# Optimization experiments

Hardware: AMD Instinct MI355X
Metric: run time of the kernel (lower is better)

The kernel has to match this reference:

```python
import jax, jax.numpy as jnp
import numpy as np

CONF_THRES = 0.1
IOU_THRES = 0.6
MAX_DET = 300
MAX_WH = 4096.0  # class offset for non-agnostic NMS
NEG_SLOPE = 0.01  # nn.LeakyReLU default


def xywh2xyxy(p):
    xy, wh = p[..., :2], p[..., 2:4]
    return jnp.concatenate([xy - wh / 2, xy + wh / 2], axis=-1)


def pairwise_iou(a, b):
    area_a = (a[:, 2] - a[:, 0]) * (a[:, 3] - a[:, 1])
    area_b = (b[:, 2] - b[:, 0]) * (b[:, 3] - b[:, 1])
    lt = jnp.maximum(a[:, None, :2], b[None, :, :2])
    rb = jnp.minimum(a[:, None, 2:], b[None, :, 2:])
    wh = jnp.clip(rb - lt, 0.0)
    inter = wh[..., 0] * wh[..., 1]
    return inter / (area_a[:, None] + area_b[None, :] - inter + 1e-7)


def nms_single(pred):  # pred: [N, 5+nc]
    boxes = xywh2xyxy(pred[:, :4])
    scores = pred[:, 5:] * pred[:, 4:5]  # obj * cls
    conf = jnp.max(scores, axis=1)
    cls = jnp.argmax(scores, axis=1)
    conf = jnp.where(conf > CONF_THRES, conf, 0.0)
    topv, topi = jax.lax.top_k(conf, MAX_DET)
    b = boxes[topi]                      # [K,4]
    c = cls[topi]
    valid = topv > CONF_THRES
    bo = b + (c.astype(b.dtype) * MAX_WH)[:, None]  # class-offset boxes
    iou = pairwise_iou(bo, bo)           # [K,K]
    idx = jnp.arange(MAX_DET)
    def body(i, keep):
        sup = keep[i] & (iou[i] > IOU_THRES) & (idx > i)
        return keep & ~sup
    keep = jax.lax.fori_loop(0, MAX_DET, body, valid)
    return b, keep


def bilinear_sample(feat, y, x):  # feat [C,H,W], y/x [K,P] -> [C,K,P]
    C, H, W = feat.shape
    y = jnp.clip(y, 0.0, H - 1.0)
    x = jnp.clip(x, 0.0, W - 1.0)
    y0 = jnp.floor(y).astype(jnp.int32)
    x0 = jnp.floor(x).astype(jnp.int32)
    y1 = jnp.minimum(y0 + 1, H - 1)
    x1 = jnp.minimum(x0 + 1, W - 1)
    ly = y - y0
    lx = x - x0
    return (feat[:, y0, x0] * ((1 - ly) * (1 - lx))
            + feat[:, y0, x1] * ((1 - ly) * lx)
            + feat[:, y1, x0] * (ly * (1 - lx))
            + feat[:, y1, x1] * (ly * lx))


def roi_align_1x1(feat, boxes, scale):  # feat [C,H,W], boxes [K,4] xyxy (input-px)
    b = boxes * scale
    w = jnp.maximum(b[:, 2] - b[:, 0], 1.0)
    h = jnp.maximum(b[:, 3] - b[:, 1], 1.0)
    off = jnp.array([0.5, 1.5], dtype=boxes.dtype)
    xs = b[:, 0:1] + off[None, :] * (w[:, None] / 2.0)  # [K,2]
    ys = b[:, 1:2] + off[None, :] * (h[:, None] / 2.0)
    yy = ys[:, jnp.array([0, 0, 1, 1])]  # [K,4] 2x2 grid
    xx = xs[:, jnp.array([0, 1, 0, 1])]
    v = bilinear_sample(feat, yy, xx)    # [C,K,4]
    return jnp.mean(v, axis=2).T         # [K,C]


def rescale_boxes(bbox, hw, hw0):  # scale_coords + normalize by orig shape
    gain = jnp.minimum(hw[0] / hw0[0], hw[1] / hw0[1])
    pad_x = (hw[1] - hw0[1] * gain) / 2.0
    pad_y = (hw[0] - hw0[0] * gain) / 2.0
    x1 = jnp.clip((bbox[:, 0] - pad_x) / gain, 0.0, hw0[1])
    y1 = jnp.clip((bbox[:, 1] - pad_y) / gain, 0.0, hw0[0])
    x2 = jnp.clip((bbox[:, 2] - pad_x) / gain, 0.0, hw0[1])
    y2 = jnp.clip((bbox[:, 3] - pad_y) / gain, 0.0, hw0[0])
    # divide by shapes[i][0] indexed [w,h,w,h]
    return jnp.stack([x1 / hw0[1], y1 / hw0[0], x2 / hw0[1], y2 / hw0[0]], axis=1)


def setup_inputs() -> dict:
    key = jax.random.key(0)
    ks = jax.random.split(key, 10)
    B, N, NC = 8, 25500, 80
    xy = jax.random.uniform(ks[0], (B, N, 2), minval=0.0, maxval=640.0)
    wh = jax.random.uniform(ks[1], (B, N, 2), minval=8.0, maxval=160.0)
    obj = jax.random.uniform(ks[2], (B, N, 1))
    cls = jax.random.uniform(ks[3], (B, N, NC))
    preds = jnp.concatenate([xy, wh, obj, cls], axis=-1)
    feat1 = jax.random.normal(ks[4], (B, 128, 80, 80), dtype=jnp.float32)
    feat2 = jax.random.normal(ks[5], (B, 256, 40, 40), dtype=jnp.float32)
    feat3 = jax.random.normal(ks[6], (B, 512, 20, 20), dtype=jnp.float32)
    feat4 = jax.random.normal(ks[7], (B, 1024, 10, 10), dtype=jnp.float32)
    orig_hw = jnp.tile(jnp.array([[720.0, 1280.0]], dtype=jnp.float32), (B, 1))
    W1 = jax.random.normal(ks[8], (1920, 256), dtype=jnp.float32) * 0.02
    b1 = jnp.zeros((256,), dtype=jnp.float32)
    W2 = jax.random.normal(ks[9], (256, 256), dtype=jnp.float32) * 0.02
    b2 = jnp.zeros((256,), dtype=jnp.float32)
    return {"preds": preds, "feat1": feat1, "feat2": feat2, "feat3": feat3,
            "feat4": feat4, "orig_hw": orig_hw, "W1": W1, "b1": b1,
            "W2": W2, "b2": b2}


def reference(preds, feat1, feat2, feat3, feat4, orig_hw, W1, b1, W2, b2):
    preds = jax.lax.stop_gradient(preds)  # out.detach() in the original
    hw = jnp.array(feat1.shape[-2:], dtype=preds.dtype) * 8.0  # network input h,w
    boxes, keep = jax.vmap(nms_single)(preds)  # [B,K,4], [B,K]
    f1 = jax.vmap(lambda f, b: roi_align_1x1(f, b, 1.0 / 8))(feat1, boxes)
    f2 = jax.vmap(lambda f, b: roi_align_1x1(f, b, 1.0 / 16))(feat2, boxes)
    f3 = jax.vmap(lambda f, b: roi_align_1x1(f, b, 1.0 / 32))(feat3, boxes)
    f4 = jax.vmap(lambda f, b: roi_align_1x1(f, b, 1.0 / 64))(feat4, boxes)
    f = jnp.concatenate([f1, f2, f3, f4], axis=-1)  # [B,K,1920]
    h = jax.nn.leaky_relu(f @ W1 + b1, NEG_SLOPE)
    h = jax.nn.leaky_relu(h @ W2 + b2, NEG_SLOPE)   # [B,K,256]
    bb = jax.vmap(lambda b, s: rescale_boxes(b, hw, s))(boxes, orig_hw)
    out = jnp.concatenate([bb, h], axis=-1)  # [B,K,260]
    return out * keep[..., None].astype(out.dtype)
```

## Files before the change

### kernel.cpp

```cpp
#include <hip/hip_runtime.h>
#include <hip/hip_bf16.h>
#include <cstdint>
#include <cstddef>

#define NBATCH 8
#define NANCH 25500
#define MAXDET 300

typedef __bf16 bf16x8 __attribute__((ext_vector_type(8)));
typedef float floatx4 __attribute__((ext_vector_type(4)));
typedef unsigned long long ull;

#define CONF_TILE 64
__global__ __launch_bounds__(256) void conf_kernel(const float* __restrict__ preds,
                                                   float* __restrict__ conf,
                                                   int* __restrict__ cls, int total) {
  __shared__ float s[CONF_TILE * 85];
  int base = blockIdx.x * CONF_TILE;
  int nA = total - base; if (nA > CONF_TILE) nA = CONF_TILE;
  int n4 = (nA * 85) >> 2;
  const float4* g4 = (const float4*)(preds + (size_t)base * 85);
  float4* s4 = (float4*)s;
  for (int i = threadIdx.x; i < n4; i += 256) s4[i] = g4[i];
  __syncthreads();
  int lane16 = threadIdx.x & 15;
  int sub = threadIdx.x >> 4;
  #pragma unroll
  for (int r = 0; r < 4; ++r) {
    int a = r * 16 + sub;
    if (a < nA) {
      const float* row = s + a * 85;
      float obj = row[4];
      float best = -1.0f; int bc = 0;
      #pragma unroll
      for (int j = 0; j < 5; ++j) {
        int c = lane16 * 5 + j;
        float v = row[5 + c] * obj;
        if (v > best) { best = v; bc = c; }
      }
      #pragma unroll
      for (int m = 1; m < 16; m <<= 1) {
        float ov = __shfl_xor(best, m, 64);
        int   oc = __shfl_xor(bc,   m, 64);
        if (ov > best || (ov == best && oc < bc)) { best = ov; bc = oc; }
      }
      if (lane16 == 0) {
        int idx = base + a;
        conf[idx] = (best > 0.1f) ? best : 0.0f;
        cls[idx] = bc;
      }
    }
  }
}

#define TK_CAP 2560
__global__ __launch_bounds__(1024) void topk_nms_kernel(const float* __restrict__ conf,
                                                        const float* __restrict__ preds,
                                                        const int* __restrict__ cls,
                                                        float* __restrict__ topv, int* __restrict__ topi,
                                                        float* __restrict__ cand_v, int* __restrict__ cand_i,
                                                        float* __restrict__ boxesWs, int* __restrict__ keepWs,
                                                        const float* __restrict__ orig_hw,
                                                        float* __restrict__ out, int N) {
  #pragma clang fp contract(off)
  __shared__ __align__(16) char smem[41216];
  int b = blockIdx.x;
  int t = threadIdx.x;

  {
    int* hist   = (int*)smem;
    int* spart  = (int*)(smem + 16384);
    float* lv_s = (float*)(smem + 20480);
    int* li_s   = (int*)(smem + 30720);
    int* shv    = (int*)(smem + 40960);
    const float* cf = conf + (size_t)b * N;
    const float4* cf4 = (const float4*)cf;
    int N4 = N >> 2;
    for (int i = t; i < 4096; i += 1024) hist[i] = 0;
    if (t == 0) { shv[0] = -1; shv[1] = 0; }
    __syncthreads();
    auto histo = [&](float v) {
      if (v > 0.1f) {
        unsigned bits = __float_as_uint(v);
        int bin = (int)((bits - 0x3D800000u) >> 13);
        if (bin > 4095) bin = 4095;
        atomicAdd(&hist[bin], 1);
      }
    };
    for (int i4 = t; i4 < N4; i4 += 1024) {
      float4 v = cf4[i4];
      histo(v.x); histo(v.y); histo(v.z); histo(v.w);
    }
    __syncthreads();
    int g = hist[4 * t] + hist[4 * t + 1] + hist[4 * t + 2] + hist[4 * t + 3];
    spart[t] = g;
    __syncthreads();
    for (int offs = 1; offs < 1024; offs <<= 1) {
      int v = (t + offs < 1024) ? spart[t + offs] : 0;
      __syncthreads();
      spart[t] += v;
      __syncthreads();
    }
    int total = spart[0];
    int target = total < 300 ? total : 300;
    if (total > 0) {
      int excl = spart[t] - g;
      int c3 = excl + hist[4 * t + 3];
      int c2 = c3 + hist[4 * t + 2];
      int c1 = c2 + hist[4 * t + 1];
      int c0 = c1 + hist[4 * t + 0];
      if      (c3 >= target) atomicMax(&shv[0], 4 * t + 3);
      else if (c2 >= target) atomicMax(&shv[0], 4 * t + 2);
      else if (c1 >= target) atomicMax(&shv[0], 4 * t + 1);
      else if (c0 >= target) atomicMax(&shv[0], 4 * t + 0);
    }
    __syncthreads();
    for (int i = t; i < 300; i += 1024) { topv[b * 300 + i] = 0.0f; topi[b * 300 + i] = 0; }
    int T = shv[0];
    float* cv = cand_v + (size_t)b * N;
    int* ci = cand_i + (size_t)b * N;
    if (total > 0) {
      auto cand = [&](float v, int idx) {
        if (v > 0.1f) {
          unsigned bits = __float_as_uint(v);
          int bin = (int)((bits - 0x3D800000u) >> 13);
          if (bin > 4095) bin = 4095;
          if (bin >= T) {
            int pos = atomicAdd(&shv[1], 1);
            if (pos < TK_CAP) { lv_s[pos] = v; li_s[pos] = idx; }
            else { cv[pos] = v; ci[pos] = idx; }
          }
        }
      };
      for (int i4 = t; i4 < N4; i4 += 1024) {
        float4 v = cf4[i4];
        int i = i4 * 4;
        cand(v.x, i); cand(v.y, i + 1); cand(v.z, i + 2); cand(v.w, i + 3);
      }
    }
    __syncthreads();
    int K = shv[1];
    int Klds = K < TK_CAP ? K : TK_CAP;
    for (int i = t; i < K; i += 1024) {
      float v; int id;
      if (i < TK_CAP) { v = lv_s[i]; id = li_s[i]; }
      else            { v = cv[i];   id = ci[i];   }
      int rank = 0;
      #pragma unroll 8
      for (int j = 0; j < Klds; ++j) {
        float vj = lv_s[j];
        int ij = li_s[j];
        int gt = vj > v;
        int eq = (vj == v) & (ij < id);
        rank += gt | eq;
      }
      for (int j = TK_CAP; j < K; ++j) {
        float vj = cv[j];
        int ij = ci[j];
        int gt = vj > v;
        int eq = (vj == v) & (ij < id);
        rank += gt | eq;
      }
      if (rank < 300) { topv[b * 300 + rank] = v; topi[b * 300 + rank] = id; }
    }
  }
  __syncthreads();

  {
    ull  (*mask)[5] = (ull(*)[5])smem;
    float (*bo5)[5] = (float(*)[5])(smem + 12032);
    float (*bxx)[4] = (float(*)[4])(smem + 18048);
    ull* keepw = (ull*)(smem + 22848);
    ull* nzrow = (ull*)(smem + 22888);
    if (t < 5) { keepw[t] = 0ULL; nzrow[t] = 0ULL; }
    __syncthreads();
    if (t < 300) {
      int i = topi[b * 300 + t];
      float v = topv[b * 300 + t];
      const float* p = preds + ((size_t)b * N + i) * 85;
      float cx = p[0], cy = p[1], w = p[2], h = p[3];
      float hw2 = w * 0.5f, hh2 = h * 0.5f;
      float x1 = cx - hw2, y1 = cy - hh2, x2 = cx + hw2, y2 = cy + hh2;
      bxx[t][0] = x1; bxx[t][1] = y1; bxx[t][2] = x2; bxx[t][3] = y2;
      size_t bi = ((size_t)(b * 300 + t)) * 4;
      boxesWs[bi + 0] = x1; boxesWs[bi + 1] = y1; boxesWs[bi + 2] = x2; boxesWs[bi + 3] = y2;
      int c = cls[(size_t)b * N + i];
      float off = (float)c * 4096.0f;
      float o0 = x1 + off, o1 = y1 + off, o2 = x2 + off, o3 = y2 + off;
      bo5[t][0] = o0; bo5[t][1] = o1; bo5[t][2] = o2; bo5[t][3] = o3;
      bo5[t][4] = (o2 - o0) * (o3 - o1);
      if (v > 0.1f) atomicOr(&keepw[t >> 6], 1ULL << (t & 63));
    }
    __syncthreads();
    {
      int wv = t >> 6, ln = t & 63;
      if (wv < 10) {
        int w = wv >> 1, half = wv & 1;
        int j = w * 64 + ln;
        int jc = j < 300 ? j : 0;
        float jb0 = bo5[jc][0], jb1 = bo5[jc][1], jb2 = bo5[jc][2], jb3 = bo5[jc][3], ja = bo5[jc][4];
        bool jv = j < 300;
        int iend = w * 64 + 64; if (iend > 300) iend = 300;
        int i0 = half * 150, i1 = i0 + 150; if (i1 > iend) i1 = iend;
        #pragma unroll 4
        for (int i = i0; i < i1; ++i) {
          float a0 = bo5[i][0], a1 = bo5[i][1], a2 = bo5[i][2], a3 = bo5[i][3], ai = bo5[i][4];
          float ltx = fmaxf(a0, jb0);
          float lty = fmaxf(a1, jb1);
          float rbx = fminf(a2, jb2);
          float rby = fminf(a3, jb3);
          float wx = fmaxf(rbx - ltx, 0.0f);
          float wy = fmaxf(rby - lty, 0.0f);
          float inter = wx * wy;
          float iou = inter / (ai + ja - inter + 1e-7f);
          ull bal = __ballot(jv && (j > i) && (iou > 0.6f));
          if (ln == 0) {
            mask[i][w] = bal;
            if (bal) atomicOr(&nzrow[i >> 6], 1ULL << (i & 63));
          }
        }
      }
    }
    __syncthreads();
    if (t == 0) {
      ull kw[5], nz[5];
      #pragma unroll
      for (int w = 0; w < 5; ++w) { kw[w] = keepw[w]; nz[w] = nzrow[w]; }
      #pragma unroll
      for (int w = 0; w < 5; ++w) {
        ull p = kw[w] & nz[w];
        while (p) {
          int l = __builtin_ctzll(p);
          p &= p - 1;
          int i = w * 64 + l;
          for (int w2 = w; w2 < 5; ++w2) {
            ull m = mask[i][w2];
            kw[w2] &= ~m;
            if (w2 == w) p &= ~m;
          }
        }
      }
      #pragma unroll
      for (int w = 0; w < 5; ++w) keepw[w] = kw[w];
    }
    __syncthreads();
    if (t < 300) {
      int kp = (int)((keepw[t >> 6] >> (t & 63)) & 1ULL);
      keepWs[b * 300 + t] = kp;
      float oh = orig_hw[b * 2 + 0], ow = orig_hw[b * 2 + 1];
      float gain = fminf(640.0f / oh, 640.0f / ow);
      float padx = (640.0f - ow * gain) * 0.5f;
      float pady = (640.0f - oh * gain) * 0.5f;
      float x1 = fminf(fmaxf((bxx[t][0] - padx) / gain, 0.0f), ow) / ow;
      float y1 = fminf(fmaxf((bxx[t][1] - pady) / gain, 0.0f), oh) / oh;
      float x2 = fminf(fmaxf((bxx[t][2] - padx) / gain, 0.0f), ow) / ow;
      float y2 = fminf(fmaxf((bxx[t][3] - pady) / gain, 0.0f), oh) / oh;
      size_t o = ((size_t)(b * 300 + t)) * 260;
      out[o + 0] = kp ? x1 : 0.0f;
      out[o + 1] = kp ? y1 : 0.0f;
      out[o + 2] = kp ? x2 : 0.0f;
      out[o + 3] = kp ? y2 : 0.0f;
    }
  }
}

struct TransArgs {
  const float* src[6];
  __hip_bfloat16* dst[6];
  int C[6], HW[6], tx[6], tpb[6], start[6];
};

__global__ void transpose_all_kernel(TransArgs a) {
  __shared__ float tile[32][33];
  int bid = blockIdx.x;
  int s = 0;
  #pragma unroll
  for (int i = 1; i < 6; ++i) if (bid >= a.start[i]) s = i;
  int local = bid - a.start[s];
  int C = a.C[s], HW = a.HW[s], tx0 = a.tx[s], tpb = a.tpb[s];
  int b = local / tpb;
  int rem = local - b * tpb;
  int p0 = (rem % tx0) * 32;
  int c0 = (rem / tx0) * 32;
  const float* inb = a.src[s] + (size_t)b * C * HW;
  __hip_bfloat16* outb = a.dst[s] + (size_t)b * C * HW;
  int tx = threadIdx.x, ty = threadIdx.y;
  #pragma unroll
  for (int k = 0; k < 32; k += 8) {
    int c = c0 + ty + k, p = p0 + tx;
    if (c < C && p < HW) tile[ty + k][tx] = inb[(size_t)c * HW + p];
  }
  __syncthreads();
  #pragma unroll
  for (int k = 0; k < 32; k += 8) {
    int p = p0 + ty + k, c = c0 + tx;
    if (p < HW && c < C) outb[(size_t)p * C + c] = __float2bfloat16(tile[tx][ty + k]);
  }
}

__global__ __launch_bounds__(256) void roi_kernel(const float* __restrict__ boxes,
                                                  const __hip_bfloat16* __restrict__ fT1, const __hip_bfloat16* __restrict__ fT2,
                                                  const __hip_bfloat16* __restrict__ fT3, const __hip_bfloat16* __restrict__ fT4,
                                                  __hip_bfloat16* __restrict__ f) {
  int b = blockIdx.x & 7;
  int r = blockIdx.x >> 3;
  __shared__ int t_off[4][16];
  __shared__ float t_w[4][16];
  int t = threadIdx.x;
  const int Hs[4] = {80, 40, 20, 10};
  const int Cs[4] = {128, 256, 512, 1024};
  const float ss[4] = {0.125f, 0.0625f, 0.03125f, 0.015625f};
  size_t bbase = ((size_t)(b * 300 + r)) * 4;
  float bx0 = boxes[bbase + 0];
  float by0 = boxes[bbase + 1];
  float bx1 = boxes[bbase + 2];
  float by1 = boxes[bbase + 3];
  if (t < 64) {
    int lv = t >> 4, k = t & 15, pp = k >> 2, nb = k & 3;
    float s = ss[lv];
    int H = Hs[lv], W = Hs[lv], C = Cs[lv];
    float b0 = bx0 * s, b1 = by0 * s, b2 = bx1 * s, b3 = by1 * s;
    float w = fmaxf(b2 - b0, 1.0f), h = fmaxf(b3 - b1, 1.0f);
    const float offv[2] = {0.5f, 1.5f};
    float px = b0 + offv[pp & 1] * (w * 0.5f);
    float py = b1 + offv[pp >> 1] * (h * 0.5f);
    float y = fminf(fmaxf(py, 0.0f), (float)(H - 1));
    float x = fminf(fmaxf(px, 0.0f), (float)(W - 1));
    int y0 = (int)floorf(y), x0 = (int)floorf(x);
    int y1 = min(y0 + 1, H - 1), x1 = min(x0 + 1, W - 1);
    float ly = y - (float)y0, lx = x - (float)x0;
    int yy = (nb & 2) ? y1 : y0;
    int xx = (nb & 1) ? x1 : x0;
    float wy = (nb & 2) ? ly : (1.0f - ly);
    float wx = (nb & 1) ? lx : (1.0f - lx);
    t_off[lv][k] = (yy * W + xx) * C;
    t_w[lv][k] = wy * wx;
  }
  __syncthreads();
  const __hip_bfloat16* bases[4] = {
    fT1 + (size_t)b * 6400 * 128,
    fT2 + (size_t)b * 1600 * 256,
    fT3 + (size_t)b * 400 * 512,
    fT4 + (size_t)b * 100 * 1024
  };
  __hip_bfloat16* frow = f + (size_t)(b * 300 + r) * 1920;
  int cbase = 0;
  #pragma unroll
  for (int lv = 0; lv < 4; ++lv) {
    int C = Cs[lv];
    const __hip_bfloat16* base = bases[lv];
    for (int c = t; c < C; c += 256) {
      float acc = 0.0f;
      #pragma unroll
      for (int k = 0; k < 16; ++k)
        acc += t_w[lv][k] * __bfloat162float(base[t_off[lv][k] + c]);
      frow[cbase + c] = __float2bfloat16(acc * 0.25f);
    }
    cbase += C;
  }
}

#define GLDS16(gp, lp) __builtin_amdgcn_global_load_lds( \
    (const __attribute__((address_space(1))) unsigned int*)(gp), \
    (__attribute__((address_space(3))) unsigned int*)(lp), 16, 0, 0)

__global__ __launch_bounds__(256) void gemm_tile_kernel(const __hip_bfloat16* __restrict__ A,
                                                        const __hip_bfloat16* __restrict__ BT,
                                                        const float* __restrict__ bias,
                                                        __hip_bfloat16* __restrict__ Cb,
                                                        float* __restrict__ Cf,
                                                        const int* __restrict__ keep,
                                                        int M, int N, int K, int ldc, int coff) {
  __shared__ __hip_bfloat16 sA[2][64 * 64];
  __shared__ __hip_bfloat16 sB[2][64 * 64];
  int tid = threadIdx.x;
  int bm = blockIdx.x * 64, bn = blockIdx.y * 64;
  int wave = tid >> 6, lane = tid & 63;
  int wr = wave >> 1, wc = wave & 1;
  int idx16 = lane & 15, kb = lane >> 4;
  floatx4 acc[2][2] = {};
  int nt = K >> 6;

  auto stage = [&](int buf, int t) {
    int k0 = t << 6;
    #pragma unroll
    for (int i = 0; i < 2; ++i) {
      int c = tid + i * 256;
      int row = c >> 3, cc = c & 7;
      int scc = cc ^ (row & 7);
      GLDS16(A + (size_t)(bm + row) * K + k0 + scc * 8,
             (char*)&sA[buf][0] + c * 16);
    }
    #pragma unroll
    for (int i = 0; i < 2; ++i) {
      int c = tid + i * 256;
      int row = c >> 3, cc = c & 7;
      int scc = cc ^ (row & 7);
      GLDS16(BT + (size_t)(bn + row) * K + k0 + scc * 8,
             (char*)&sB[buf][0] + c * 16);
    }
  };

  stage(0, 0);
  asm volatile("s_waitcnt vmcnt(0)" ::: "memory");
  __syncthreads();
  int cur = 0;
  for (int t = 0; t < nt; ++t) {
    if (t + 1 < nt) stage(cur ^ 1, t + 1);
    const char* Ab = (const char*)&sA[cur][0];
    const char* Bb = (const char*)&sB[cur][0];
    #pragma unroll
    for (int s = 0; s < 2; ++s) {
      bf16x8 af[2], bg[2];
      #pragma unroll
      for (int m = 0; m < 2; ++m) {
        int row = wr * 32 + m * 16 + idx16;
        int chunk = s * 4 + kb;
        af[m] = *(const bf16x8*)(Ab + row * 128 + ((chunk ^ (row & 7)) * 16));
      }
      #pragma unroll
      for (int n = 0; n < 2; ++n) {
        int row = wc * 32 + n * 16 + idx16;
        int chunk = s * 4 + kb;
        bg[n] = *(const bf16x8*)(Bb + row * 128 + ((chunk ^ (row & 7)) * 16));
      }
      #pragma unroll
      for (int m = 0; m < 2; ++m)
        #pragma unroll
        for (int n = 0; n < 2; ++n)
          acc[m][n] = __builtin_amdgcn_mfma_f32_16x16x32_bf16(af[m], bg[n], acc[m][n], 0, 0, 0);
    }
    asm volatile("s_waitcnt vmcnt(0)" ::: "memory");
    __syncthreads();
    cur ^= 1;
  }
  int col = lane & 15, rb4 = (lane >> 4) * 4;
  #pragma unroll
  for (int m = 0; m < 2; ++m) {
    #pragma unroll
    for (int n = 0; n < 2; ++n) {
      #pragma unroll
      for (int r = 0; r < 4; ++r) {
        int orow = bm + wr * 32 + m * 16 + rb4 + r;
        int ocol = bn + wc * 32 + n * 16 + col;
        if (orow >= M) continue;
        float v = acc[m][n][r] + bias[ocol];
        v = (v >= 0.0f) ? v : 0.01f * v;
        if (Cb) Cb[(size_t)orow * N + ocol] = __float2bfloat16(v);
        if (Cf) {
          float km = keep ? (keep[orow] ? 1.0f : 0.0f) : 1.0f;
          Cf[(size_t)orow * ldc + coff + ocol] = v * km;
        }
      }
    }
  }
}

extern "C" void kernel_launch(void* const* d_in, const int* in_sizes, int n_in,
                              void* d_out, int out_size, void* d_ws, size_t ws_size,
                              hipStream_t stream) {
  (void)in_sizes; (void)n_in; (void)out_size; (void)ws_size;
  const float* preds  = (const float*)d_in[0];
  const float* feat1  = (const float*)d_in[1];
  const float* feat2  = (const float*)d_in[2];
  const float* feat3  = (const float*)d_in[3];
  const float* feat4  = (const float*)d_in[4];
  const float* orighw = (const float*)d_in[5];
  const float* W1     = (const float*)d_in[6];
  const float* b1     = (const float*)d_in[7];
  const float* W2     = (const float*)d_in[8];
  const float* b2     = (const float*)d_in[9];
  float* out = (float*)d_out;

  char* ws = (char*)d_ws;
  size_t off = 0;
  auto alloc = [&](size_t bytes) -> void* {
    void* p = ws + off;
    off = (off + bytes + 255) & ~(size_t)255;
    return p;
  };
  const int BN = NBATCH * NANCH;
  float* conf   = (float*)alloc((size_t)BN * 4);
  int*   cls    = (int*)  alloc((size_t)BN * 4);
  float* cand_v = (float*)alloc((size_t)BN * 4);
  int*   cand_i = (int*)  alloc((size_t)BN * 4);
  float* topv   = (float*)alloc((size_t)NBATCH * 300 * 4);
  int*   topi   = (int*)  alloc((size_t)NBATCH * 300 * 4);
  float* boxes  = (float*)alloc((size_t)NBATCH * 300 * 4 * 4);
  int*   keep   = (int*)  alloc((size_t)NBATCH * 300 * 4);
  __hip_bfloat16* fT1  = (__hip_bfloat16*)alloc((size_t)NBATCH * 6400 * 128 * 2);
  __hip_bfloat16* fT2  = (__hip_bfloat16*)alloc((size_t)NBATCH * 1600 * 256 * 2);
  __hip_bfloat16* fT3  = (__hip_bfloat16*)alloc((size_t)NBATCH * 400 * 512 * 2);
  __hip_bfloat16* fT4  = (__hip_bfloat16*)alloc((size_t)NBATCH * 100 * 1024 * 2);
  __hip_bfloat16* fmat = (__hip_bfloat16*)alloc((size_t)2400 * 1920 * 2);
  __hip_bfloat16* h1b  = (__hip_bfloat16*)alloc((size_t)2400 * 256 * 2);
  __hip_bfloat16* W1T  = (__hip_bfloat16*)alloc((size_t)256 * 1920 * 2);
  __hip_bfloat16* W2T  = (__hip_bfloat16*)alloc((size_t)256 * 256 * 2);

  conf_kernel<<<(BN + CONF_TILE - 1) / CONF_TILE, 256, 0, stream>>>(preds, conf, cls, BN);
  topk_nms_kernel<<<NBATCH, 1024, 0, stream>>>(conf, preds, cls, topv, topi, cand_v, cand_i,
                                               boxes, keep, orighw, out, NANCH);
  TransArgs ta;
  ta.src[0] = feat1; ta.dst[0] = fT1; ta.C[0] = 128;  ta.HW[0] = 6400; ta.tx[0] = 200;
  ta.src[1] = feat2; ta.dst[1] = fT2; ta.C[1] = 256;  ta.HW[1] = 1600; ta.tx[1] = 50;
  ta.src[2] = feat3; ta.dst[2] = fT3; ta.C[2] = 512;  ta.HW[2] = 400;  ta.tx[2] = 13;
  ta.src[3] = feat4; ta.dst[3] = fT4; ta.C[3] = 1024; ta.HW[3] = 100;  ta.tx[3] = 4;
  ta.src[4] = W1;    ta.dst[4] = W1T; ta.C[4] = 1920; ta.HW[4] = 256;  ta.tx[4] = 8;
  ta.src[5] = W2;    ta.dst[5] = W2T; ta.C[5] = 256;  ta.HW[5] = 256;  ta.tx[5] = 8;
  int total_blocks = 0;
  for (int s = 0; s < 6; ++s) {
    int ty = (ta.C[s] + 31) / 32;
    int nbatch = (s < 4) ? NBATCH : 1;
    ta.tpb[s] = ta.tx[s] * ty;
    ta.start[s] = total_blocks;
    total_blocks += ta.tpb[s] * nbatch;
  }
  transpose_all_kernel<<<total_blocks, dim3(32, 8), 0, stream>>>(ta);
  roi_kernel<<<2400, 256, 0, stream>>>(boxes, fT1, fT2, fT3, fT4, fmat);
  gemm_tile_kernel<<<dim3(38, 4), 256, 0, stream>>>(fmat, W1T, b1, h1b, nullptr, nullptr,
                                                    2400, 256, 1920, 0, 0);
  gemm_tile_kernel<<<dim3(38, 4), 256, 0, stream>>>(h1b, W2T, b2, nullptr, out, keep,
                                                    2400, 256, 256, 260, 4);
}
```

Before: 142.5 us.

## Move top-k histogram into parallel blocks of transpose kernel, coarsen bins

The confidence histogram used for top-k threshold selection is now built by 64 extra blocks added to the transpose kernel (8 segments per batch), which accumulate into a global 512-bin histogram via atomics. The top-k/NMS kernel then only loads that histogram and does a wave-shuffle suffix scan, replacing the 4096-bin in-kernel histogram and the barrier-heavy scan. Top-k values and indices now stay in shared memory instead of a global scratch round trip. Coarser bins can admit more candidates for the rank pass, and TK_CAP is lowered to 2048, so more candidates may spill to global memory. The change also adds a memset launch.

```diff
diff --git a/kernel.cpp b/kernel.cpp
--- a/kernel.cpp
+++ b/kernel.cpp
@@ -53,78 +53,75 @@
   }
 }
 
-#define TK_CAP 2560
+#define TK_CAP 2048
 __global__ __launch_bounds__(1024) void topk_nms_kernel(const float* __restrict__ conf,
                                                         const float* __restrict__ preds,
                                                         const int* __restrict__ cls,
-                                                        float* __restrict__ topv, int* __restrict__ topi,
+                                                        const int* __restrict__ ghist,
                                                         float* __restrict__ cand_v, int* __restrict__ cand_i,
                                                         float* __restrict__ boxesWs, int* __restrict__ keepWs,
                                                         const float* __restrict__ orig_hw,
                                                         float* __restrict__ out, int N) {
   #pragma clang fp contract(off)
-  __shared__ __align__(16) char smem[41216];
+  __shared__ __align__(16) char smem[43008];
   int b = blockIdx.x;
   int t = threadIdx.x;
 
+  int*   s_h  = (int*)smem;
+  int*   s_c  = (int*)(smem + 2048);
+  float* tv   = (float*)(smem + 23040);
+  int*   ti   = (int*)(smem + 24256);
+  float* lv_s = (float*)(smem + 25600);
+  int*   li_s = (int*)(smem + 33792);
+  int*   shv  = (int*)(smem + 41984);
+
+  int T, total;
   {
-    int* hist   = (int*)smem;
-    int* spart  = (int*)(smem + 16384);
-    float* lv_s = (float*)(smem + 20480);
-    int* li_s   = (int*)(smem + 30720);
-    int* shv    = (int*)(smem + 40960);
+    if (t == 0) shv[1] = 0;
+    if (t < 512) s_h[t] = ghist[b * 512 + t];
+    for (int i = t; i < 300; i += 1024) { tv[i] = 0.0f; ti[i] = 0; }
+    __syncthreads();
+    int suff = 0;
+    if (t < 512) {
+      suff = s_h[t];
+      int l = t & 63;
+      #pragma unroll
+      for (int d = 1; d < 64; d <<= 1) {
+        int o = __shfl_down(suff, d, 64);
+        if (l + d < 64) suff += o;
+      }
+    }
+    __syncthreads();
+    if (t < 512 && (t & 63) == 0) s_h[t >> 6] = suff;
+    __syncthreads();
+    if (t < 512) {
+      int w = t >> 6;
+      int hi = 0;
+      #pragma unroll
+      for (int w2 = 1; w2 < 8; ++w2) if (w2 > w) hi += s_h[w2];
+      s_c[t] = suff + hi;
+    }
+    __syncthreads();
+    total = s_c[0];
+    int target = total < 300 ? total : 300;
+    if (t < 512) {
+      int c = s_c[t];
+      if (c >= target && (t == 511 || s_c[t + 1] < target)) shv[0] = t;
+    }
+    __syncthreads();
+    T = shv[0];
+
     const float* cf = conf + (size_t)b * N;
     const float4* cf4 = (const float4*)cf;
     int N4 = N >> 2;
-    for (int i = t; i < 4096; i += 1024) hist[i] = 0;
-    if (t == 0) { shv[0] = -1; shv[1] = 0; }
-    __syncthreads();
-    auto histo = [&](float v) {
-      if (v > 0.1f) {
-        unsigned bits = __float_as_uint(v);
-        int bin = (int)((bits - 0x3D800000u) >> 13);
-        if (bin > 4095) bin = 4095;
-        atomicAdd(&hist[bin], 1);
-      }
-    };
-    for (int i4 = t; i4 < N4; i4 += 1024) {
-      float4 v = cf4[i4];
-      histo(v.x); histo(v.y); histo(v.z); histo(v.w);
-    }
-    __syncthreads();
-    int g = hist[4 * t] + hist[4 * t + 1] + hist[4 * t + 2] + hist[4 * t + 3];
-    spart[t] = g;
-    __syncthreads();
-    for (int offs = 1; offs < 1024; offs <<= 1) {
-      int v = (t + offs < 1024) ? spart[t + offs] : 0;
-      __syncthreads();
-      spart[t] += v;
-      __syncthreads();
-    }
-    int total = spart[0];
-    int target = total < 300 ? total : 300;
-    if (total > 0) {
-      int excl = spart[t] - g;
-      int c3 = excl + hist[4 * t + 3];
-      int c2 = c3 + hist[4 * t + 2];
-      int c1 = c2 + hist[4 * t + 1];
-      int c0 = c1 + hist[4 * t + 0];
-      if      (c3 >= target) atomicMax(&shv[0], 4 * t + 3);
-      else if (c2 >= target) atomicMax(&shv[0], 4 * t + 2);
-      else if (c1 >= target) atomicMax(&shv[0], 4 * t + 1);
-      else if (c0 >= target) atomicMax(&shv[0], 4 * t + 0);
-    }
-    __syncthreads();
-    for (int i = t; i < 300; i += 1024) { topv[b * 300 + i] = 0.0f; topi[b * 300 + i] = 0; }
-    int T = shv[0];
     float* cv = cand_v + (size_t)b * N;
     int* ci = cand_i + (size_t)b * N;
     if (total > 0) {
       auto cand = [&](float v, int idx) {
         if (v > 0.1f) {
           unsigned bits = __float_as_uint(v);
-          int bin = (int)((bits - 0x3D800000u) >> 13);
-          if (bin > 4095) bin = 4095;
+          int bin = (int)((bits - 0x3D800000u) >> 16);
+          if (bin > 511) bin = 511;
           if (bin >= T) {
             int pos = atomicAdd(&shv[1], 1);
             if (pos < TK_CAP) { lv_s[pos] = v; li_s[pos] = idx; }
@@ -161,7 +158,7 @@
         int eq = (vj == v) & (ij < id);
         rank += gt | eq;
       }
-      if (rank < 300) { topv[b * 300 + rank] = v; topi[b * 300 + rank] = id; }
+      if (rank < 300) { tv[rank] = v; ti[rank] = id; }
     }
   }
   __syncthreads();
@@ -175,8 +172,8 @@
     if (t < 5) { keepw[t] = 0ULL; nzrow[t] = 0ULL; }
     __syncthreads();
     if (t < 300) {
-      int i = topi[b * 300 + t];
-      float v = topv[b * 300 + t];
+      int i = ti[t];
+      float v = tv[t];
       const float* p = preds + ((size_t)b * N + i) * 85;
       float cx = p[0], cy = p[1], w = p[2], h = p[3];
       float hw2 = w * 0.5f, hh2 = h * 0.5f;
@@ -270,9 +267,39 @@
   int C[6], HW[6], tx[6], tpb[6], start[6];
 };
 
-__global__ void transpose_all_kernel(TransArgs a) {
-  __shared__ float tile[32][33];
+__global__ void transpose_all_kernel(TransArgs a, const float* __restrict__ conf,
+                                     int* __restrict__ ghist, int hist_start) {
+  __shared__ __align__(16) char msm[4352];
   int bid = blockIdx.x;
+  if (bid >= hist_start) {
+    int* sh = (int*)msm;
+    int hb = bid - hist_start;
+    int b = hb >> 3, seg = hb & 7;
+    int tid = threadIdx.y * 32 + threadIdx.x;
+    sh[tid] = 0; sh[tid + 256] = 0;
+    __syncthreads();
+    const int N4 = NANCH >> 2;
+    int i0 = (N4 * seg) >> 3, i1 = (N4 * (seg + 1)) >> 3;
+    const float4* cf4 = (const float4*)(conf + (size_t)b * NANCH);
+    auto histo = [&](float v) {
+      if (v > 0.1f) {
+        unsigned bits = __float_as_uint(v);
+        int bin = (int)((bits - 0x3D800000u) >> 16);
+        if (bin > 511) bin = 511;
+        atomicAdd(&sh[bin], 1);
+      }
+    };
+    for (int i = i0 + tid; i < i1; i += 256) {
+      float4 v = cf4[i];
+      histo(v.x); histo(v.y); histo(v.z); histo(v.w);
+    }
+    __syncthreads();
+    int c0 = sh[tid], c1 = sh[tid + 256];
+    if (c0) atomicAdd(&ghist[b * 512 + tid], c0);
+    if (c1) atomicAdd(&ghist[b * 512 + tid + 256], c1);
+    return;
+  }
+  float (*tile)[33] = (float(*)[33])msm;
   int s = 0;
   #pragma unroll
   for (int i = 1; i < 6; ++i) if (bid >= a.start[i]) s = i;
@@ -484,8 +511,7 @@
   int*   cls    = (int*)  alloc((size_t)BN * 4);
   float* cand_v = (float*)alloc((size_t)BN * 4);
   int*   cand_i = (int*)  alloc((size_t)BN * 4);
-  float* topv   = (float*)alloc((size_t)NBATCH * 300 * 4);
-  int*   topi   = (int*)  alloc((size_t)NBATCH * 300 * 4);
+  int*   ghist  = (int*)  alloc((size_t)NBATCH * 512 * 4);
   float* boxes  = (float*)alloc((size_t)NBATCH * 300 * 4 * 4);
   int*   keep   = (int*)  alloc((size_t)NBATCH * 300 * 4);
   __hip_bfloat16* fT1  = (__hip_bfloat16*)alloc((size_t)NBATCH * 6400 * 128 * 2);
@@ -497,9 +523,10 @@
   __hip_bfloat16* W1T  = (__hip_bfloat16*)alloc((size_t)256 * 1920 * 2);
   __hip_bfloat16* W2T  = (__hip_bfloat16*)alloc((size_t)256 * 256 * 2);
 
+  hipMemsetAsync(ghist, 0, (size_t)NBATCH * 512 * 4, stream);
+
   conf_kernel<<<(BN + CONF_TILE - 1) / CONF_TILE, 256, 0, stream>>>(preds, conf, cls, BN);
-  topk_nms_kernel<<<NBATCH, 1024, 0, stream>>>(conf, preds, cls, topv, topi, cand_v, cand_i,
-                                               boxes, keep, orighw, out, NANCH);
+
   TransArgs ta;
   ta.src[0] = feat1; ta.dst[0] = fT1; ta.C[0] = 128;  ta.HW[0] = 6400; ta.tx[0] = 200;
   ta.src[1] = feat2; ta.dst[1] = fT2; ta.C[1] = 256;  ta.HW[1] = 1600; ta.tx[1] = 50;
@@ -515,7 +542,10 @@
     ta.start[s] = total_blocks;
     total_blocks += ta.tpb[s] * nbatch;
   }
-  transpose_all_kernel<<<total_blocks, dim3(32, 8), 0, stream>>>(ta);
+  transpose_all_kernel<<<total_blocks + 64, dim3(32, 8), 0, stream>>>(ta, conf, ghist, total_blocks);
+
+  topk_nms_kernel<<<NBATCH, 1024, 0, stream>>>(conf, preds, cls, ghist, cand_v, cand_i,
+                                               boxes, keep, orighw, out, NANCH);
   roi_kernel<<<2400, 256, 0, stream>>>(boxes, fT1, fT2, fT3, fT4, fmat);
   gemm_tile_kernel<<<dim3(38, 4), 256, 0, stream>>>(fmat, W1T, b1, h1b, nullptr, nullptr,
                                                     2400, 256, 1920, 0, 0);
```

Result: no change. 144.3 us (+1.2%).

## Overlap top-k candidate selection with transposes and bucket candidates by histogram bin

Applied to the files above, without the earlier changes.

The 8-block histogram/threshold/candidate-gather stage moves into the first blocks of the transpose kernel, so it runs alongside the feature and weight transposes instead of as a serial 8-block launch. Candidates are scattered into bin-sorted slots using suffix-sum counters, and each candidate's box and class are gathered at that point. Ranking then only compares against entries in the same bin instead of all candidates. The histogram becomes coarser (2048 bins), which can enlarge the threshold bin, and the scatter costs extra global writes of boxes and classes.

```diff
diff --git a/kernel.cpp b/kernel.cpp
--- a/kernel.cpp
+++ b/kernel.cpp
@@ -6,10 +6,17 @@
 #define NBATCH 8
 #define NANCH 25500
 #define MAXDET 300
+#define NBINS 2048
 
 typedef __bf16 bf16x8 __attribute__((ext_vector_type(8)));
 typedef float floatx4 __attribute__((ext_vector_type(4)));
 typedef unsigned long long ull;
+
+__device__ __forceinline__ int conf_bin(float v) {
+  unsigned bits = __float_as_uint(v);
+  int bin = (int)((bits - 0x3D800000u) >> 14);
+  return bin > (NBINS - 1) ? (NBINS - 1) : bin;
+}
 
 #define CONF_TILE 64
 __global__ __launch_bounds__(256) void conf_kernel(const float* __restrict__ preds,
@@ -53,226 +60,112 @@
   }
 }
 
-#define TK_CAP 2560
-__global__ __launch_bounds__(1024) void topk_nms_kernel(const float* __restrict__ conf,
-                                                        const float* __restrict__ preds,
-                                                        const int* __restrict__ cls,
-                                                        float* __restrict__ topv, int* __restrict__ topi,
-                                                        float* __restrict__ cand_v, int* __restrict__ cand_i,
-                                                        float* __restrict__ boxesWs, int* __restrict__ keepWs,
-                                                        const float* __restrict__ orig_hw,
-                                                        float* __restrict__ out, int N) {
-  #pragma clang fp contract(off)
-  __shared__ __align__(16) char smem[41216];
-  int b = blockIdx.x;
-  int t = threadIdx.x;
-
-  {
-    int* hist   = (int*)smem;
-    int* spart  = (int*)(smem + 16384);
-    float* lv_s = (float*)(smem + 20480);
-    int* li_s   = (int*)(smem + 30720);
-    int* shv    = (int*)(smem + 40960);
-    const float* cf = conf + (size_t)b * N;
-    const float4* cf4 = (const float4*)cf;
-    int N4 = N >> 2;
-    for (int i = t; i < 4096; i += 1024) hist[i] = 0;
-    if (t == 0) { shv[0] = -1; shv[1] = 0; }
-    __syncthreads();
-    auto histo = [&](float v) {
-      if (v > 0.1f) {
-        unsigned bits = __float_as_uint(v);
-        int bin = (int)((bits - 0x3D800000u) >> 13);
-        if (bin > 4095) bin = 4095;
-        atomicAdd(&hist[bin], 1);
-      }
-    };
-    for (int i4 = t; i4 < N4; i4 += 1024) {
-      float4 v = cf4[i4];
-      histo(v.x); histo(v.y); histo(v.z); histo(v.w);
-    }
-    __syncthreads();
-    int g = hist[4 * t] + hist[4 * t + 1] + hist[4 * t + 2] + hist[4 * t + 3];
-    spart[t] = g;
-    __syncthreads();
-    for (int offs = 1; offs < 1024; offs <<= 1) {
-      int v = (t + offs < 1024) ? spart[t + offs] : 0;
-      __syncthreads();
-      spart[t] += v;
-      __syncthreads();
-    }
-    int total = spart[0];
-    int target = total < 300 ? total : 300;
-    if (total > 0) {
-      int excl = spart[t] - g;
-      int c3 = excl + hist[4 * t + 3];
-      int c2 = c3 + hist[4 * t + 2];
-      int c1 = c2 + hist[4 * t + 1];
-      int c0 = c1 + hist[4 * t + 0];
-      if      (c3 >= target) atomicMax(&shv[0], 4 * t + 3);
-      else if (c2 >= target) atomicMax(&shv[0], 4 * t + 2);
-      else if (c1 >= target) atomicMax(&shv[0], 4 * t + 1);
-      else if (c0 >= target) atomicMax(&shv[0], 4 * t + 0);
-    }
-    __syncthreads();
-    for (int i = t; i < 300; i += 1024) { topv[b * 300 + i] = 0.0f; topi[b * 300 + i] = 0; }
-    int T = shv[0];
-    float* cv = cand_v + (size_t)b * N;
-    int* ci = cand_i + (size_t)b * N;
-    if (total > 0) {
-      auto cand = [&](float v, int idx) {
-        if (v > 0.1f) {
-          unsigned bits = __float_as_uint(v);
-          int bin = (int)((bits - 0x3D800000u) >> 13);
-          if (bin > 4095) bin = 4095;
-          if (bin >= T) {
-            int pos = atomicAdd(&shv[1], 1);
-            if (pos < TK_CAP) { lv_s[pos] = v; li_s[pos] = idx; }
-            else { cv[pos] = v; ci[pos] = idx; }
-          }
-        }
-      };
-      for (int i4 = t; i4 < N4; i4 += 1024) {
-        float4 v = cf4[i4];
-        int i = i4 * 4;
-        cand(v.x, i); cand(v.y, i + 1); cand(v.z, i + 2); cand(v.w, i + 3);
-      }
-    }
-    __syncthreads();
-    int K = shv[1];
-    int Klds = K < TK_CAP ? K : TK_CAP;
-    for (int i = t; i < K; i += 1024) {
-      float v; int id;
-      if (i < TK_CAP) { v = lv_s[i]; id = li_s[i]; }
-      else            { v = cv[i];   id = ci[i];   }
-      int rank = 0;
-      #pragma unroll 8
-      for (int j = 0; j < Klds; ++j) {
-        float vj = lv_s[j];
-        int ij = li_s[j];
-        int gt = vj > v;
-        int eq = (vj == v) & (ij < id);
-        rank += gt | eq;
-      }
-      for (int j = TK_CAP; j < K; ++j) {
-        float vj = cv[j];
-        int ij = ci[j];
-        int gt = vj > v;
-        int eq = (vj == v) & (ij < id);
-        rank += gt | eq;
-      }
-      if (rank < 300) { topv[b * 300 + rank] = v; topi[b * 300 + rank] = id; }
-    }
-  }
-  __syncthreads();
-
-  {
-    ull  (*mask)[5] = (ull(*)[5])smem;
-    float (*bo5)[5] = (float(*)[5])(smem + 12032);
-    float (*bxx)[4] = (float(*)[4])(smem + 18048);
-    ull* keepw = (ull*)(smem + 22848);
-    ull* nzrow = (ull*)(smem + 22888);
-    if (t < 5) { keepw[t] = 0ULL; nzrow[t] = 0ULL; }
-    __syncthreads();
-    if (t < 300) {
-      int i = topi[b * 300 + t];
-      float v = topv[b * 300 + t];
-      const float* p = preds + ((size_t)b * N + i) * 85;
-      float cx = p[0], cy = p[1], w = p[2], h = p[3];
-      float hw2 = w * 0.5f, hh2 = h * 0.5f;
-      float x1 = cx - hw2, y1 = cy - hh2, x2 = cx + hw2, y2 = cy + hh2;
-      bxx[t][0] = x1; bxx[t][1] = y1; bxx[t][2] = x2; bxx[t][3] = y2;
-      size_t bi = ((size_t)(b * 300 + t)) * 4;
-      boxesWs[bi + 0] = x1; boxesWs[bi + 1] = y1; boxesWs[bi + 2] = x2; boxesWs[bi + 3] = y2;
-      int c = cls[(size_t)b * N + i];
-      float off = (float)c * 4096.0f;
-      float o0 = x1 + off, o1 = y1 + off, o2 = x2 + off, o3 = y2 + off;
-      bo5[t][0] = o0; bo5[t][1] = o1; bo5[t][2] = o2; bo5[t][3] = o3;
-      bo5[t][4] = (o2 - o0) * (o3 - o1);
-      if (v > 0.1f) atomicOr(&keepw[t >> 6], 1ULL << (t & 63));
-    }
-    __syncthreads();
-    {
-      int wv = t >> 6, ln = t & 63;
-      if (wv < 10) {
-        int w = wv >> 1, half = wv & 1;
-        int j = w * 64 + ln;
-        int jc = j < 300 ? j : 0;
-        float jb0 = bo5[jc][0], jb1 = bo5[jc][1], jb2 = bo5[jc][2], jb3 = bo5[jc][3], ja = bo5[jc][4];
-        bool jv = j < 300;
-        int iend = w * 64 + 64; if (iend > 300) iend = 300;
-        int i0 = half * 150, i1 = i0 + 150; if (i1 > iend) i1 = iend;
-        #pragma unroll 4
-        for (int i = i0; i < i1; ++i) {
-          float a0 = bo5[i][0], a1 = bo5[i][1], a2 = bo5[i][2], a3 = bo5[i][3], ai = bo5[i][4];
-          float ltx = fmaxf(a0, jb0);
-          float lty = fmaxf(a1, jb1);
-          float rbx = fminf(a2, jb2);
-          float rby = fminf(a3, jb3);
-          float wx = fmaxf(rbx - ltx, 0.0f);
-          float wy = fmaxf(rby - lty, 0.0f);
-          float inter = wx * wy;
-          float iou = inter / (ai + ja - inter + 1e-7f);
-          ull bal = __ballot(jv && (j > i) && (iou > 0.6f));
-          if (ln == 0) {
-            mask[i][w] = bal;
-            if (bal) atomicOr(&nzrow[i >> 6], 1ULL << (i & 63));
-          }
-        }
-      }
-    }
-    __syncthreads();
-    if (t == 0) {
-      ull kw[5], nz[5];
-      #pragma unroll
-      for (int w = 0; w < 5; ++w) { kw[w] = keepw[w]; nz[w] = nzrow[w]; }
-      #pragma unroll
-      for (int w = 0; w < 5; ++w) {
-        ull p = kw[w] & nz[w];
-        while (p) {
-          int l = __builtin_ctzll(p);
-          p &= p - 1;
-          int i = w * 64 + l;
-          for (int w2 = w; w2 < 5; ++w2) {
-            ull m = mask[i][w2];
-            kw[w2] &= ~m;
-            if (w2 == w) p &= ~m;
-          }
-        }
-      }
-      #pragma unroll
-      for (int w = 0; w < 5; ++w) keepw[w] = kw[w];
-    }
-    __syncthreads();
-    if (t < 300) {
-      int kp = (int)((keepw[t >> 6] >> (t & 63)) & 1ULL);
-      keepWs[b * 300 + t] = kp;
-      float oh = orig_hw[b * 2 + 0], ow = orig_hw[b * 2 + 1];
-      float gain = fminf(640.0f / oh, 640.0f / ow);
-      float padx = (640.0f - ow * gain) * 0.5f;
-      float pady = (640.0f - oh * gain) * 0.5f;
-      float x1 = fminf(fmaxf((bxx[t][0] - padx) / gain, 0.0f), ow) / ow;
-      float y1 = fminf(fmaxf((bxx[t][1] - pady) / gain, 0.0f), oh) / oh;
-      float x2 = fminf(fmaxf((bxx[t][2] - padx) / gain, 0.0f), ow) / ow;
-      float y2 = fminf(fmaxf((bxx[t][3] - pady) / gain, 0.0f), oh) / oh;
-      size_t o = ((size_t)(b * 300 + t)) * 260;
-      out[o + 0] = kp ? x1 : 0.0f;
-      out[o + 1] = kp ? y1 : 0.0f;
-      out[o + 2] = kp ? x2 : 0.0f;
-      out[o + 3] = kp ? y2 : 0.0f;
-    }
-  }
-}
-
 struct TransArgs {
   const float* src[6];
   __hip_bfloat16* dst[6];
   int C[6], HW[6], tx[6], tpb[6], start[6];
 };
 
-__global__ void transpose_all_kernel(TransArgs a) {
-  __shared__ float tile[32][33];
+__global__ void transpose_all_kernel(TransArgs a,
+                                     const float* __restrict__ conf,
+                                     const float* __restrict__ preds,
+                                     const int* __restrict__ clsg,
+                                     float2* __restrict__ svid,
+                                     float4* __restrict__ sbox,
+                                     int* __restrict__ scls,
+                                     int* __restrict__ sufG,
+                                     int* __restrict__ tinfo) {
+  __shared__ __align__(16) char msm[17536];
   int bid = blockIdx.x;
+  if (bid < NBATCH) {
+    #pragma clang fp contract(off)
+    int b = bid;
+    int tid = threadIdx.y * 32 + threadIdx.x;
+    int* s_h   = (int*)msm;
+    int* s_ctr = (int*)(msm + 8192);
+    int* s_p   = (int*)(msm + 16384);
+    int* shv   = (int*)(msm + 17408);
+    for (int i = tid; i < NBINS; i += 256) s_h[i] = 0;
+    __syncthreads();
+    const float* cf = conf + (size_t)b * NANCH;
+    const float4* cf4 = (const float4*)cf;
+    const int N4 = NANCH >> 2;
+    for (int i = tid; i < N4; i += 256) {
+      float4 v = cf4[i];
+      if (v.x > 0.1f) atomicAdd(&s_h[conf_bin(v.x)], 1);
+      if (v.y > 0.1f) atomicAdd(&s_h[conf_bin(v.y)], 1);
+      if (v.z > 0.1f) atomicAdd(&s_h[conf_bin(v.z)], 1);
+      if (v.w > 0.1f) atomicAdd(&s_h[conf_bin(v.w)], 1);
+    }
+    __syncthreads();
+    int base = tid * 8;
+    int vals[8]; int ctot = 0;
+    #pragma unroll
+    for (int k = 0; k < 8; ++k) { vals[k] = s_h[base + k]; ctot += vals[k]; }
+    s_p[tid] = ctot;
+    __syncthreads();
+    for (int off = 1; off < 256; off <<= 1) {
+      int v = (tid + off < 256) ? s_p[tid + off] : 0;
+      __syncthreads();
+      s_p[tid] += v;
+      __syncthreads();
+    }
+    int total = s_p[0];
+    int above = (tid < 255) ? s_p[tid + 1] : 0;
+    int run = above;
+    #pragma unroll
+    for (int k = 7; k >= 0; --k) { run += vals[k]; s_h[base + k] = run; }
+    if (tid == 0) { sufG[b * (NBINS + 1) + NBINS] = 0; shv[0] = NBINS; }
+    __syncthreads();
+    int target = total < 300 ? total : 300;
+    int* sg = sufG + b * (NBINS + 1);
+    #pragma unroll
+    for (int k = 0; k < 8; ++k) {
+      int bin = base + k;
+      int sv = s_h[bin];
+      int nx = (bin < NBINS - 1) ? s_h[bin + 1] : 0;
+      s_ctr[bin] = nx;
+      sg[bin] = sv;
+      if (total > 0 && sv >= target && nx < target) shv[0] = bin;
+    }
+    __syncthreads();
+    int T = shv[0];
+    if (tid == 0) {
+      tinfo[b * 2 + 0] = total;
+      tinfo[b * 2 + 1] = (T < NBINS) ? s_h[T] : 0;
+    }
+    if (total > 0) {
+      float2* vb = svid + (size_t)b * NANCH;
+      float4* bb = sbox + (size_t)b * NANCH;
+      int*    cb = scls + (size_t)b * NANCH;
+      for (int i4 = tid; i4 < N4; i4 += 256) {
+        float4 v4 = cf4[i4];
+        int i0 = i4 * 4;
+        float vv[4] = {v4.x, v4.y, v4.z, v4.w};
+        #pragma unroll
+        for (int q = 0; q < 4; ++q) {
+          float v = vv[q];
+          if (v > 0.1f) {
+            int bin = conf_bin(v);
+            if (bin >= T) {
+              int slot = atomicAdd(&s_ctr[bin], 1);
+              int idx = i0 + q;
+              const float* p = preds + ((size_t)b * NANCH + idx) * 85;
+              float cx = p[0], cy = p[1], w = p[2], h = p[3];
+              float hw2 = w * 0.5f, hh2 = h * 0.5f;
+              float2 vi; vi.x = v; vi.y = __int_as_float(idx);
+              vb[slot] = vi;
+              float4 bx; bx.x = cx - hw2; bx.y = cy - hh2; bx.z = cx + hw2; bx.w = cy + hh2;
+              bb[slot] = bx;
+              cb[slot] = clsg[(size_t)b * NANCH + idx];
+            }
+          }
+        }
+      }
+    }
+    return;
+  }
+  float (*tile)[33] = (float(*)[33])msm;
   int s = 0;
   #pragma unroll
   for (int i = 1; i < 6; ++i) if (bid >= a.start[i]) s = i;
@@ -295,6 +188,149 @@
   for (int k = 0; k < 32; k += 8) {
     int p = p0 + ty + k, c = c0 + tx;
     if (p < HW && c < C) outb[(size_t)p * C + c] = __float2bfloat16(tile[tx][ty + k]);
+  }
+}
+
+__global__ __launch_bounds__(1024) void nms_kernel(const float2* __restrict__ svid,
+                                                   const float4* __restrict__ sbox,
+                                                   const int* __restrict__ scls,
+                                                   const int* __restrict__ sufG,
+                                                   const int* __restrict__ tinfo,
+                                                   float* __restrict__ boxesWs, int* __restrict__ keepWs,
+                                                   const float* __restrict__ orig_hw,
+                                                   float* __restrict__ out) {
+  #pragma clang fp contract(off)
+  __shared__ float4 bo4[300];
+  __shared__ float bxx[300][4];
+  __shared__ ull mask[300][5];
+  __shared__ ull keepw[5];
+  __shared__ ull nzrow[5];
+  int b = blockIdx.x;
+  int t = threadIdx.x;
+  int total  = tinfo[b * 2 + 0];
+  int Kslots = tinfo[b * 2 + 1];
+  int nvalid = total < 300 ? total : 300;
+
+  if (t < 300) {
+    bo4[t] = make_float4(0.0f, 0.0f, 0.0f, 0.0f);
+    bxx[t][0] = 0.0f; bxx[t][1] = 0.0f; bxx[t][2] = 0.0f; bxx[t][3] = 0.0f;
+    if (t >= nvalid) {
+      size_t bi = ((size_t)(b * 300 + t)) * 4;
+      boxesWs[bi + 0] = 0.0f; boxesWs[bi + 1] = 0.0f;
+      boxesWs[bi + 2] = 0.0f; boxesWs[bi + 3] = 0.0f;
+    }
+  }
+  if (t < 5) {
+    int kbase = t * 64;
+    int n = nvalid - kbase;
+    keepw[t] = (n <= 0) ? 0ULL : (n >= 64 ? ~0ULL : ((1ULL << n) - 1ULL));
+    nzrow[t] = 0ULL;
+  }
+  __syncthreads();
+
+  {
+    const float2* vb = svid + (size_t)b * NANCH;
+    const float4* bb = sbox + (size_t)b * NANCH;
+    const int*    cb = scls + (size_t)b * NANCH;
+    const int*   suf = sufG + b * (NBINS + 1);
+    for (int sIdx = t; sIdx < Kslots; sIdx += 1024) {
+      float2 vi = vb[sIdx];
+      float v = vi.x;
+      int id = __float_as_int(vi.y);
+      int bin = conf_bin(v);
+      int lo = suf[bin + 1], hi = suf[bin];
+      int rank = lo;
+      for (int j = lo; j < hi; ++j) {
+        float2 o = vb[j];
+        float vj = o.x;
+        int ij = __float_as_int(o.y);
+        rank += (int)((vj > v) | ((vj == v) & (ij < id)));
+      }
+      if (rank < 300) {
+        float4 bx = bb[sIdx];
+        int c = cb[sIdx];
+        float off = (float)c * 4096.0f;
+        float4 ob; ob.x = bx.x + off; ob.y = bx.y + off; ob.z = bx.z + off; ob.w = bx.w + off;
+        bo4[rank] = ob;
+        bxx[rank][0] = bx.x; bxx[rank][1] = bx.y; bxx[rank][2] = bx.z; bxx[rank][3] = bx.w;
+        size_t bi = ((size_t)(b * 300 + rank)) * 4;
+        boxesWs[bi + 0] = bx.x; boxesWs[bi + 1] = bx.y;
+        boxesWs[bi + 2] = bx.z; boxesWs[bi + 3] = bx.w;
+      }
+    }
+  }
+  __syncthreads();
+
+  {
+    int wv = t >> 6, ln = t & 63;
+    if (wv < 10) {
+      int w = wv >> 1, half = wv & 1;
+      int j = w * 64 + ln;
+      int jc = j < 300 ? j : 0;
+      float4 jb = bo4[jc];
+      float ja = (jb.z - jb.x) * (jb.w - jb.y);
+      bool jv = j < 300;
+      int iend = w * 64 + 64; if (iend > 300) iend = 300;
+      int i0 = half * 150, i1 = i0 + 150; if (i1 > iend) i1 = iend;
+      #pragma unroll 4
+      for (int i = i0; i < i1; ++i) {
+        float4 ib = bo4[i];
+        float ai = (ib.z - ib.x) * (ib.w - ib.y);
+        float ltx = fmaxf(ib.x, jb.x);
+        float lty = fmaxf(ib.y, jb.y);
+        float rbx = fminf(ib.z, jb.z);
+        float rby = fminf(ib.w, jb.w);
+        float wx = fmaxf(rbx - ltx, 0.0f);
+        float wy = fmaxf(rby - lty, 0.0f);
+        float inter = wx * wy;
+        float iou = inter / (ai + ja - inter + 1e-7f);
+        ull bal = __ballot(jv && (j > i) && (iou > 0.6f));
+        if (ln == 0) {
+          mask[i][w] = bal;
+          if (bal) atomicOr(&nzrow[i >> 6], 1ULL << (i & 63));
+        }
+      }
+    }
+  }
+  __syncthreads();
+  if (t == 0) {
+    ull kw[5], nz[5];
+    #pragma unroll
+    for (int w = 0; w < 5; ++w) { kw[w] = keepw[w]; nz[w] = nzrow[w]; }
+    #pragma unroll
+    for (int w = 0; w < 5; ++w) {
+      ull p = kw[w] & nz[w];
+      while (p) {
+        int l = __builtin_ctzll(p);
+        p &= p - 1;
+        int i = w * 64 + l;
+        for (int w2 = w; w2 < 5; ++w2) {
+          ull m = mask[i][w2];
+          kw[w2] &= ~m;
+          if (w2 == w) p &= ~m;
+        }
+      }
+    }
+    #pragma unroll
+    for (int w = 0; w < 5; ++w) keepw[w] = kw[w];
+  }
+  __syncthreads();
+  if (t < 300) {
+    int kp = (int)((keepw[t >> 6] >> (t & 63)) & 1ULL);
+    keepWs[b * 300 + t] = kp;
+    float oh = orig_hw[b * 2 + 0], ow = orig_hw[b * 2 + 1];
+    float gain = fminf(640.0f / oh, 640.0f / ow);
+    float padx = (640.0f - ow * gain) * 0.5f;
+    float pady = (640.0f - oh * gain) * 0.5f;
+    float x1 = fminf(fmaxf((bxx[t][0] - padx) / gain, 0.0f), ow) / ow;
+    float y1 = fminf(fmaxf((bxx[t][1] - pady) / gain, 0.0f), oh) / oh;
+    float x2 = fminf(fmaxf((bxx[t][2] - padx) / gain, 0.0f), ow) / ow;
+    float y2 = fminf(fmaxf((bxx[t][3] - pady) / gain, 0.0f), oh) / oh;
+    size_t o = ((size_t)(b * 300 + t)) * 260;
+    out[o + 0] = kp ? x1 : 0.0f;
+    out[o + 1] = kp ? y1 : 0.0f;
+    out[o + 2] = kp ? x2 : 0.0f;
+    out[o + 3] = kp ? y2 : 0.0f;
   }
 }
 
@@ -480,14 +516,15 @@
     return p;
   };
   const int BN = NBATCH * NANCH;
-  float* conf   = (float*)alloc((size_t)BN * 4);
-  int*   cls    = (int*)  alloc((size_t)BN * 4);
-  float* cand_v = (float*)alloc((size_t)BN * 4);
-  int*   cand_i = (int*)  alloc((size_t)BN * 4);
-  float* topv   = (float*)alloc((size_t)NBATCH * 300 * 4);
-  int*   topi   = (int*)  alloc((size_t)NBATCH * 300 * 4);
-  float* boxes  = (float*)alloc((size_t)NBATCH * 300 * 4 * 4);
-  int*   keep   = (int*)  alloc((size_t)NBATCH * 300 * 4);
+  float*  conf  = (float*)alloc((size_t)BN * 4);
+  int*    cls   = (int*)  alloc((size_t)BN * 4);
+  float2* svid  = (float2*)alloc((size_t)BN * 8);
+  float4* sbox  = (float4*)alloc((size_t)BN * 16);
+  int*    scls  = (int*)  alloc((size_t)BN * 4);
+  int*    sufG  = (int*)  alloc((size_t)NBATCH * (NBINS + 1) * 4);
+  int*    tinfo = (int*)  alloc((size_t)NBATCH * 2 * 4);
+  float*  boxes = (float*)alloc((size_t)NBATCH * 300 * 4 * 4);
+  int*    keep  = (int*)  alloc((size_t)NBATCH * 300 * 4);
   __hip_bfloat16* fT1  = (__hip_bfloat16*)alloc((size_t)NBATCH * 6400 * 128 * 2);
   __hip_bfloat16* fT2  = (__hip_bfloat16*)alloc((size_t)NBATCH * 1600 * 256 * 2);
   __hip_bfloat16* fT3  = (__hip_bfloat16*)alloc((size_t)NBATCH * 400 * 512 * 2);
@@ -498,8 +535,7 @@
   __hip_bfloat16* W2T  = (__hip_bfloat16*)alloc((size_t)256 * 256 * 2);
 
   conf_kernel<<<(BN + CONF_TILE - 1) / CONF_TILE, 256, 0, stream>>>(preds, conf, cls, BN);
-  topk_nms_kernel<<<NBATCH, 1024, 0, stream>>>(conf, preds, cls, topv, topi, cand_v, cand_i,
-                                               boxes, keep, orighw, out, NANCH);
+
   TransArgs ta;
   ta.src[0] = feat1; ta.dst[0] = fT1; ta.C[0] = 128;  ta.HW[0] = 6400; ta.tx[0] = 200;
   ta.src[1] = feat2; ta.dst[1] = fT2; ta.C[1] = 256;  ta.HW[1] = 1600; ta.tx[1] = 50;
@@ -507,7 +543,7 @@
   ta.src[3] = feat4; ta.dst[3] = fT4; ta.C[3] = 1024; ta.HW[3] = 100;  ta.tx[3] = 4;
   ta.src[4] = W1;    ta.dst[4] = W1T; ta.C[4] = 1920; ta.HW[4] = 256;  ta.tx[4] = 8;
   ta.src[5] = W2;    ta.dst[5] = W2T; ta.C[5] = 256;  ta.HW[5] = 256;  ta.tx[5] = 8;
-  int total_blocks = 0;
+  int total_blocks = NBATCH;
   for (int s = 0; s < 6; ++s) {
     int ty = (ta.C[s] + 31) / 32;
     int nbatch = (s < 4) ? NBATCH : 1;
@@ -515,7 +551,11 @@
     ta.start[s] = total_blocks;
     total_blocks += ta.tpb[s] * nbatch;
   }
-  transpose_all_kernel<<<total_blocks, dim3(32, 8), 0, stream>>>(ta);
+  transpose_all_kernel<<<total_blocks, dim3(32, 8), 0, stream>>>(ta, conf, preds, cls,
+                                                                 svid, sbox, scls, sufG, tinfo);
+
+  nms_kernel<<<NBATCH, 1024, 0, stream>>>(svid, sbox, scls, sufG, tinfo,
+                                          boxes, keep, orighw, out);
   roi_kernel<<<2400, 256, 0, stream>>>(boxes, fT1, fT2, fT3, fT4, fmat);
   gemm_tile_kernel<<<dim3(38, 4), 256, 0, stream>>>(fmat, W1T, b1, h1b, nullptr, nullptr,
                                                     2400, 256, 1920, 0, 0);
```

Result: slower. 154.6 us (+8.5%).
